# Kernel tuning notes

Measured on AMD Instinct MI355X. Metric: run time of the kernel, lower is better.

## Reference

```python
import jax, jax.numpy as jnp
import numpy as np

N_NODES = 100000
N_EDGES = 6400000


def setup_inputs() -> dict:
    key = jax.random.key(0)
    k1, k2, k3, k4, k5, k6 = jax.random.split(key, 6)
    x = jax.random.normal(k1, (N_NODES, 20), dtype=jnp.float32)
    edge_index = jax.random.randint(k2, (2, N_EDGES), 0, N_NODES, dtype=jnp.int64)
    # Glorot-style init for GCNConv weights, zero bias (PyG default)
    W1 = jax.random.normal(k3, (20, 16), dtype=jnp.float32) * (1.0 / np.sqrt(20))
    b1 = jnp.zeros((16,), dtype=jnp.float32)
    W2 = jax.random.normal(k4, (16, 2), dtype=jnp.float32) * (1.0 / np.sqrt(16))
    b2 = jnp.zeros((2,), dtype=jnp.float32)
    return {"x": x, "edge_index": edge_index, "W1": W1, "b1": b1, "W2": W2, "b2": b2}


def gcn_conv(x, row, col, W, b, num_nodes):
    # x' = D^{-1/2} (A + I) D^{-1/2} X W + b  (PyG GCNConv with self-loops)
    xw = x @ W  # [N, out]
    ones = jnp.ones_like(row, dtype=xw.dtype)
    deg = jax.ops.segment_sum(ones, row, num_segments=num_nodes)  # [N]
    dinv = jnp.where(deg > 0, jax.lax.rsqrt(deg), 0.0)
    norm = dinv[row] * dinv[col]  # [E+N]
    msg = xw[col] * norm[:, None]  # gather + scale
    out = jax.ops.segment_sum(msg, row, num_segments=num_nodes)  # scatter-add
    return out + b


def reference(x, edge_index, W1, b1, W2, b2):
    num_nodes = x.shape[0]
    self_loops = jnp.arange(num_nodes, dtype=edge_index.dtype)
    row = jnp.concatenate([edge_index[0], self_loops])  # target nodes
    col = jnp.concatenate([edge_index[1], self_loops])  # source nodes
    h = gcn_conv(x, row, col, W1, b1, num_nodes)
    h = jax.nn.relu(h)
    # F.dropout(x, training=self.training): identity in eval mode
    h = gcn_conv(h, row, col, W2, b2, num_nodes)
    return jax.nn.log_softmax(h, axis=1)
```

## Files before the change

### kernel.cpp

```cpp
#include <hip/hip_runtime.h>
#include <math.h>


#define XF 20
#define F1 16
#define F2 2
#define RPB 128
#define KMAX 800
#define KP   784
#define TILE 8192
#define EPT 16
#define NJMAX 800
#define CAP 9216
#define BPAD 16

__device__ __forceinline__ unsigned bf16rne(float f) {
    unsigned u = __float_as_uint(f);
    return (u + 0x7FFFu + ((u >> 16) & 1u)) >> 16;
}
__device__ __forceinline__ float bflo(unsigned w) { return __uint_as_float(w << 16); }
__device__ __forceinline__ float bfhi(unsigned w) { return __uint_as_float(w & 0xFFFF0000u); }

__global__ __launch_bounds__(512) void passA_kernel(const int* __restrict__ rows,
                                                    const int* __restrict__ cols,
                                                    int* __restrict__ bhist,
                                                    int* __restrict__ lbt,
                                                    unsigned int* __restrict__ csrtmp,
                                                    int E, int K) {
    __shared__ unsigned int stage[TILE];
    __shared__ int hist[KMAX];
    __shared__ int tsum[512];
    int t = threadIdx.x;
    int bj = blockIdx.x;
    for (int k = t; k < K; k += 512) hist[k] = 0;
    __syncthreads();
    int e0 = bj * TILE;
    int e1 = min(e0 + TILE, E);
    int n = e1 - e0;
    int rloc[EPT];
    #pragma unroll
    for (int it = 0; it < EPT; it++) {
        int e = e0 + it * 512 + t;
        if (e < e1) {
            int r = rows[e];
            rloc[it] = r;
            atomicAdd(&hist[r >> 7], 1);
        }
    }
    __syncthreads();
    int k0 = 2 * t, k1 = 2 * t + 1;
    int v0 = (k0 < K) ? hist[k0] : 0;
    int v1 = (k1 < K) ? hist[k1] : 0;
    int s = v0 + v1;
    tsum[t] = s;
    __syncthreads();
    for (int d = 1; d < 512; d <<= 1) {
        int u = (t >= d) ? tsum[t - d] : 0;
        __syncthreads();
        tsum[t] += u;
        __syncthreads();
    }
    int run = tsum[t] - s;
    long long lrow = (long long)bj * KP;
    if (k0 < K) {
        hist[k0] = run;  lbt[lrow + k0] = run;
        if (v0) atomicAdd(&bhist[k0 * BPAD], v0);
    }
    if (k1 < K) {
        hist[k1] = run + v0;  lbt[lrow + k1] = run + v0;
        if (v1) atomicAdd(&bhist[k1 * BPAD], v1);
    }
    if (t == 0) lbt[lrow + K] = n;
    __syncthreads();
    #pragma unroll
    for (int it = 0; it < EPT; it++) {
        int e = e0 + it * 512 + t;
        if (e < e1) {
            int r = rloc[it];
            int c = cols[e];
            int pos = atomicAdd(&hist[r >> 7], 1);
            stage[pos] = ((unsigned int)c << 7) | (unsigned int)(r & 127);
        }
    }
    __syncthreads();
    for (int ss = t; ss < n; ss += 512)
        csrtmp[(size_t)e0 + ss] = stage[ss];
}

__global__ void bscan_kernel(const int* __restrict__ bhist, int K, int E,
                             int* __restrict__ bbase) {
    __shared__ int tsum[256];
    int t = threadIdx.x;
    int vals[4];
    int s = 0;
    #pragma unroll
    for (int j = 0; j < 4; j++) {
        int idx = t * 4 + j;
        vals[j] = (idx < K) ? bhist[idx * BPAD] : 0;
        s += vals[j];
    }
    tsum[t] = s;
    __syncthreads();
    for (int d = 1; d < 256; d <<= 1) {
        int u = (t >= d) ? tsum[t - d] : 0;
        __syncthreads();
        tsum[t] += u;
        __syncthreads();
    }
    int run = tsum[t] - s;
    #pragma unroll
    for (int j = 0; j < 4; j++) {
        int idx = t * 4 + j;
        if (idx < K) bbase[idx] = run;
        run += vals[j];
    }
    if (t == 0) bbase[K] = E;
}

__global__ __launch_bounds__(512) void passB_kernel(const int* __restrict__ lbt,
                                                    const unsigned int* __restrict__ csrtmp,
                                                    const int* __restrict__ bbase,
                                                    unsigned int* __restrict__ csr,
                                                    int* __restrict__ rowptr,
                                                    float* __restrict__ dinv,
                                                    int N, int K, int E, int nj) {
    __shared__ unsigned int stage[CAP];
    __shared__ int segoff[NJMAX];
    __shared__ int stagepos[NJMAX + 1];
    __shared__ int dcnt[RPB];
    __shared__ int rp[RPB];
    __shared__ int cur[RPB];
    __shared__ int tsum[512];
    int b = blockIdx.x, t = threadIdx.x;
    int lo = b << 7;
    if (t < RPB) { dcnt[t] = 0; cur[t] = 0; }
    int a0 = 2 * t, a1 = 2 * t + 1;
    int la = 0, lb2 = 0;
    if (a0 < nj) {
        const int* lp = lbt + (long long)a0 * KP + b;
        int o0 = lp[0], o1 = lp[1];
        segoff[a0] = o0; la = o1 - o0;
    }
    if (a1 < nj) {
        const int* lp = lbt + (long long)a1 * KP + b;
        int o0 = lp[0], o1 = lp[1];
        segoff[a1] = o0; lb2 = o1 - o0;
    }
    int s = la + lb2;
    tsum[t] = s;
    __syncthreads();
    for (int d = 1; d < 512; d <<= 1) {
        int u = (t >= d) ? tsum[t - d] : 0;
        __syncthreads();
        tsum[t] += u;
        __syncthreads();
    }
    int run = tsum[t] - s;
    if (a0 < nj) stagepos[a0] = run;
    if (a1 < nj) stagepos[a1] = run + la;
    if (t == 511) stagepos[nj] = tsum[511];
    __syncthreads();
    int cnt = min(stagepos[nj], CAP);
    int sw = t >> 3, ln = t & 7;
    for (int seg = sw; seg < nj; seg += 64) {
        int sp = stagepos[seg];
        int len = stagepos[seg + 1] - sp;
        if (sp + len > CAP) len = max(0, CAP - sp);
        size_t src = (size_t)seg * TILE + segoff[seg];
        for (int e2 = ln; e2 < len; e2 += 8) {
            unsigned int p = csrtmp[src + e2];
            stage[sp + e2] = p;
            atomicAdd(&dcnt[p & 127u], 1);
        }
    }
    __syncthreads();
    int gb = bbase[b];
    if (t < 64) {
        int v0 = dcnt[2 * t], v1 = dcnt[2 * t + 1];
        int ss = v0 + v1;
        int sc = ss;
        #pragma unroll
        for (int d = 1; d < 64; d <<= 1) {
            int u = __shfl_up(sc, d);
            if (t >= d) sc += u;
        }
        int excl = gb + sc - ss;
        rp[2 * t] = excl;
        rp[2 * t + 1] = excl + v0;
        int i0 = lo + 2 * t, i1 = i0 + 1;
        if (i0 < N) { rowptr[i0] = excl;      dinv[i0] = rsqrtf((float)v0 + 1.0f); }
        if (i1 < N) { rowptr[i1] = excl + v0; dinv[i1] = rsqrtf((float)v1 + 1.0f); }
        if (t == 0 && b == K - 1) rowptr[N] = E;
    }
    __syncthreads();
    for (int ss = t; ss < cnt; ss += 512) {
        unsigned int p = stage[ss];
        int rr = (int)(p & 127u);
        int dst = rp[rr] + atomicAdd(&cur[rr], 1);
        csr[dst] = p >> 7;
    }
}

__global__ void xw1_kernel(const float* __restrict__ x, const float* __restrict__ W1,
                           const float* __restrict__ dinv, unsigned int* __restrict__ y1h,
                           int N) {
    __shared__ float Ws[XF * F1];
    for (int k = threadIdx.x; k < XF * F1; k += blockDim.x) Ws[k] = W1[k];
    __syncthreads();
    int i = blockIdx.x * blockDim.x + threadIdx.x;
    if (i >= N) return;
    const float4* xv = (const float4*)(x + (size_t)i * XF);
    float xr[XF];
    #pragma unroll
    for (int q = 0; q < 5; q++) {
        float4 v = xv[q];
        xr[q*4+0] = v.x; xr[q*4+1] = v.y; xr[q*4+2] = v.z; xr[q*4+3] = v.w;
    }
    float d = dinv[i];
    float out[F1];
    #pragma unroll
    for (int j = 0; j < F1; j++) {
        float a = 0.f;
        #pragma unroll
        for (int k = 0; k < XF; k++) a += xr[k] * Ws[k * F1 + j];
        out[j] = a * d;
    }
    unsigned int w[8];
    #pragma unroll
    for (int q = 0; q < 8; q++)
        w[q] = bf16rne(out[2*q]) | (bf16rne(out[2*q+1]) << 16);
    uint4* o = (uint4*)(y1h + (size_t)i * 8);
    o[0] = make_uint4(w[0], w[1], w[2], w[3]);
    o[1] = make_uint4(w[4], w[5], w[6], w[7]);
}

__global__ __launch_bounds__(256) void gather16_kernel(const int* __restrict__ rowptr,
                                                       const unsigned int* __restrict__ csr,
                                                       const unsigned int* __restrict__ y1h,
                                                       const float* __restrict__ dinv,
                                                       const float* __restrict__ b1,
                                                       const float* __restrict__ W2,
                                                       float* __restrict__ y2, int N) {
    __shared__ float W2s[F1 * F2];
    if (threadIdx.x < F1 * F2) W2s[threadIdx.x] = W2[threadIdx.x];
    __syncthreads();
    int sub = threadIdx.x >> 5;
    int l = threadIdx.x & 31;
    int i = blockIdx.x * 8 + sub;
    if (i >= N) return;
    int half = l & 1, es = l >> 1;
    int start = rowptr[i], end = rowptr[i + 1];
    const uint4* Y = (const uint4*)y1h;
    float acc[8] = {0.f, 0.f, 0.f, 0.f, 0.f, 0.f, 0.f, 0.f};
    for (int slot = start + es; slot < end; slot += 16) {
        int c = (int)csr[slot];
        uint4 w = Y[(size_t)c * 2 + half];
        acc[0] += bflo(w.x); acc[1] += bfhi(w.x);
        acc[2] += bflo(w.y); acc[3] += bfhi(w.y);
        acc[4] += bflo(w.z); acc[5] += bfhi(w.z);
        acc[6] += bflo(w.w); acc[7] += bfhi(w.w);
    }
    #pragma unroll
    for (int m = 2; m <= 16; m <<= 1) {
        #pragma unroll
        for (int k = 0; k < 8; k++) acc[k] += __shfl_xor(acc[k], m);
    }
    if (l < 2) {
        float d = dinv[i];
        uint4 w = Y[(size_t)i * 2 + l];
        float self[8] = { bflo(w.x), bfhi(w.x), bflo(w.y), bfhi(w.y),
                          bflo(w.z), bfhi(w.z), bflo(w.w), bfhi(w.w) };
        float4 bl = ((const float4*)b1)[l * 2];
        float4 bh = ((const float4*)b1)[l * 2 + 1];
        float bb[8] = { bl.x, bl.y, bl.z, bl.w, bh.x, bh.y, bh.z, bh.w };
        float p0 = 0.f, p1 = 0.f;
        #pragma unroll
        for (int k = 0; k < 8; k++) {
            float hv = fmaxf(d * (acc[k] + self[k]) + bb[k], 0.f);
            p0 += hv * W2s[(l * 8 + k) * 2];
            p1 += hv * W2s[(l * 8 + k) * 2 + 1];
        }
        float q0 = __shfl_xor(p0, 1);
        float q1 = __shfl_xor(p1, 1);
        if (l == 0)
            ((float2*)y2)[i] = make_float2((p0 + q0) * d, (p1 + q1) * d);
    }
}

__global__ __launch_bounds__(256) void gather2_kernel(const int* __restrict__ rowptr,
                                                      const unsigned int* __restrict__ csr,
                                                      const float* __restrict__ y2,
                                                      const float* __restrict__ dinv,
                                                      const float* __restrict__ b2,
                                                      float* __restrict__ out, int N) {
    int sub = threadIdx.x >> 5;
    int l = threadIdx.x & 31;
    int i = blockIdx.x * 8 + sub;
    if (i >= N) return;
    int start = rowptr[i], end = rowptr[i + 1];
    float a0 = 0.f, a1 = 0.f;
    for (int slot = start + l; slot < end; slot += 32) {
        int c = (int)csr[slot];
        float2 v = ((const float2*)y2)[c];
        a0 += v.x;
        a1 += v.y;
    }
    #pragma unroll
    for (int m = 16; m > 0; m >>= 1) {
        a0 += __shfl_xor(a0, m);
        a1 += __shfl_xor(a1, m);
    }
    if (l == 0) {
        float d = dinv[i];
        float2 yi = ((const float2*)y2)[i];
        float v0 = d * (a0 + yi.x) + b2[0];
        float v1 = d * (a1 + yi.y) + b2[1];
        float mm = fmaxf(v0, v1);
        float lse = mm + logf(expf(v0 - mm) + expf(v1 - mm));
        ((float2*)out)[i] = make_float2(v0 - lse, v1 - lse);
    }
}

static inline size_t align256(size_t x) { return (x + 255) & ~(size_t)255; }

extern "C" void kernel_launch(void* const* d_in, const int* in_sizes, int n_in,
                              void* d_out, int out_size, void* d_ws, size_t ws_size,
                              hipStream_t stream) {
    const float* x  = (const float*)d_in[0];
    const int*   ei = (const int*)d_in[1];
    const float* W1 = (const float*)d_in[2];
    const float* b1 = (const float*)d_in[3];
    const float* W2 = (const float*)d_in[4];
    const float* b2 = (const float*)d_in[5];
    float* out = (float*)d_out;

    const int N = in_sizes[0] / XF;
    const int E = in_sizes[1] / 2;
    const int* rows = ei;
    const int* cols = ei + E;
    const int K = (N + RPB - 1) >> 7;
    const int nj = (E + TILE - 1) / TILE;

    char* ws = (char*)d_ws;
    size_t off = 0;
    int*   bhist   = (int*)(ws + off);   off = align256(off + (size_t)KMAX * BPAD * 4);
    size_t zero_bytes = off;
    int*   bbase   = (int*)(ws + off);   off = align256(off + (size_t)(KMAX + 1) * 4);
    int*   rowptr  = (int*)(ws + off);   off = align256(off + (size_t)(N + 1) * 4);
    float* dinv    = (float*)(ws + off); off = align256(off + (size_t)N * 4);
    int*   lbt     = (int*)(ws + off);   off = align256(off + (size_t)nj * KP * 4);
    unsigned int* csr = (unsigned int*)(ws + off); off = align256(off + (size_t)E * 4);
    size_t tmp0 = off;
    unsigned int* csrtmp = (unsigned int*)(ws + tmp0);
    unsigned int* y1h = (unsigned int*)(ws + tmp0);
    float* y2 = (float*)(ws + align256(tmp0 + (size_t)N * 8 * 4));

    hipMemsetAsync(d_ws, 0, zero_bytes, stream);

    const int B = 256;
    const int nbN = (N + B - 1) / B;
    const int nbW = (N + 7) / 8;

    passA_kernel<<<nj, 512, 0, stream>>>(rows, cols, bhist, lbt, csrtmp, E, K);
    bscan_kernel<<<1, B, 0, stream>>>(bhist, K, E, bbase);
    passB_kernel<<<K, 512, 0, stream>>>(lbt, csrtmp, bbase, csr, rowptr, dinv, N, K, E, nj);
    xw1_kernel<<<nbN, B, 0, stream>>>(x, W1, dinv, y1h, N);
    gather16_kernel<<<nbW, B, 0, stream>>>(rowptr, csr, y1h, dinv, b1, W2, y2, N);
    gather2_kernel<<<nbW, B, 0, stream>>>(rowptr, csr, y2, dinv, b2, out, N);
}
```

Baseline: 278.7 us.

## Drop global bucket scan by using fixed per-bucket CSR slots and start/end row pairs

Removes the bucket histogram atomics, the single-block bscan kernel and the memset by giving every 128-row bucket a fixed CAP-sized slot in the CSR array, with rows addressed through (start,end) int2 pairs. passA now uses 1024-thread blocks over 16384-edge tiles, which halves the number of tiles that passB has to merge. Both gather kernels prefetch the next column index one iteration ahead. The cost is a padded CSR buffer, and it depends on no bucket ever holding more than CAP edges, which the random test inputs satisfy.

```diff
diff --git a/kernel.cpp b/kernel.cpp
--- a/kernel.cpp
+++ b/kernel.cpp
@@ -8,11 +8,10 @@
 #define RPB 128
 #define KMAX 800
 #define KP   784
-#define TILE 8192
+#define TILE 16384
 #define EPT 16
-#define NJMAX 800
+#define NJMAX 400
 #define CAP 9216
-#define BPAD 16
 
 __device__ __forceinline__ unsigned bf16rne(float f) {
     unsigned u = __float_as_uint(f);
@@ -21,18 +20,17 @@
 __device__ __forceinline__ float bflo(unsigned w) { return __uint_as_float(w << 16); }
 __device__ __forceinline__ float bfhi(unsigned w) { return __uint_as_float(w & 0xFFFF0000u); }
 
-__global__ __launch_bounds__(512) void passA_kernel(const int* __restrict__ rows,
-                                                    const int* __restrict__ cols,
-                                                    int* __restrict__ bhist,
-                                                    int* __restrict__ lbt,
-                                                    unsigned int* __restrict__ csrtmp,
-                                                    int E, int K) {
+__global__ __launch_bounds__(1024, 8) void passA_kernel(const int* __restrict__ rows,
+                                                        const int* __restrict__ cols,
+                                                        int* __restrict__ lbt,
+                                                        unsigned int* __restrict__ csrtmp,
+                                                        int E, int K) {
     __shared__ unsigned int stage[TILE];
     __shared__ int hist[KMAX];
-    __shared__ int tsum[512];
+    __shared__ int tsum[1024];
     int t = threadIdx.x;
     int bj = blockIdx.x;
-    for (int k = t; k < K; k += 512) hist[k] = 0;
+    for (int k = t; k < K; k += 1024) hist[k] = 0;
     __syncthreads();
     int e0 = bj * TILE;
     int e1 = min(e0 + TILE, E);
@@ -40,7 +38,7 @@
     int rloc[EPT];
     #pragma unroll
     for (int it = 0; it < EPT; it++) {
-        int e = e0 + it * 512 + t;
+        int e = e0 + it * 1024 + t;
         if (e < e1) {
             int r = rows[e];
             rloc[it] = r;
@@ -48,33 +46,23 @@
         }
     }
     __syncthreads();
-    int k0 = 2 * t, k1 = 2 * t + 1;
-    int v0 = (k0 < K) ? hist[k0] : 0;
-    int v1 = (k1 < K) ? hist[k1] : 0;
-    int s = v0 + v1;
-    tsum[t] = s;
-    __syncthreads();
-    for (int d = 1; d < 512; d <<= 1) {
+    int v = (t < K) ? hist[t] : 0;
+    tsum[t] = v;
+    __syncthreads();
+    for (int d = 1; d < 1024; d <<= 1) {
         int u = (t >= d) ? tsum[t - d] : 0;
         __syncthreads();
         tsum[t] += u;
         __syncthreads();
     }
-    int run = tsum[t] - s;
+    int run = tsum[t] - v;
     long long lrow = (long long)bj * KP;
-    if (k0 < K) {
-        hist[k0] = run;  lbt[lrow + k0] = run;
-        if (v0) atomicAdd(&bhist[k0 * BPAD], v0);
-    }
-    if (k1 < K) {
-        hist[k1] = run + v0;  lbt[lrow + k1] = run + v0;
-        if (v1) atomicAdd(&bhist[k1 * BPAD], v1);
-    }
+    if (t < K) { hist[t] = run; lbt[lrow + t] = run; }
     if (t == 0) lbt[lrow + K] = n;
     __syncthreads();
     #pragma unroll
     for (int it = 0; it < EPT; it++) {
-        int e = e0 + it * 512 + t;
+        int e = e0 + it * 1024 + t;
         if (e < e1) {
             int r = rloc[it];
             int c = cols[e];
@@ -83,47 +71,16 @@
         }
     }
     __syncthreads();
-    for (int ss = t; ss < n; ss += 512)
+    for (int ss = t; ss < n; ss += 1024)
         csrtmp[(size_t)e0 + ss] = stage[ss];
-}
-
-__global__ void bscan_kernel(const int* __restrict__ bhist, int K, int E,
-                             int* __restrict__ bbase) {
-    __shared__ int tsum[256];
-    int t = threadIdx.x;
-    int vals[4];
-    int s = 0;
-    #pragma unroll
-    for (int j = 0; j < 4; j++) {
-        int idx = t * 4 + j;
-        vals[j] = (idx < K) ? bhist[idx * BPAD] : 0;
-        s += vals[j];
-    }
-    tsum[t] = s;
-    __syncthreads();
-    for (int d = 1; d < 256; d <<= 1) {
-        int u = (t >= d) ? tsum[t - d] : 0;
-        __syncthreads();
-        tsum[t] += u;
-        __syncthreads();
-    }
-    int run = tsum[t] - s;
-    #pragma unroll
-    for (int j = 0; j < 4; j++) {
-        int idx = t * 4 + j;
-        if (idx < K) bbase[idx] = run;
-        run += vals[j];
-    }
-    if (t == 0) bbase[K] = E;
 }
 
 __global__ __launch_bounds__(512) void passB_kernel(const int* __restrict__ lbt,
                                                     const unsigned int* __restrict__ csrtmp,
-                                                    const int* __restrict__ bbase,
                                                     unsigned int* __restrict__ csr,
-                                                    int* __restrict__ rowptr,
+                                                    int2* __restrict__ rp2,
                                                     float* __restrict__ dinv,
-                                                    int N, int K, int E, int nj) {
+                                                    int N, int K, int nj) {
     __shared__ unsigned int stage[CAP];
     __shared__ int segoff[NJMAX];
     __shared__ int stagepos[NJMAX + 1];
@@ -134,20 +91,13 @@
     int b = blockIdx.x, t = threadIdx.x;
     int lo = b << 7;
     if (t < RPB) { dcnt[t] = 0; cur[t] = 0; }
-    int a0 = 2 * t, a1 = 2 * t + 1;
-    int la = 0, lb2 = 0;
-    if (a0 < nj) {
-        const int* lp = lbt + (long long)a0 * KP + b;
+    int la = 0;
+    if (t < nj) {
+        const int* lp = lbt + (long long)t * KP + b;
         int o0 = lp[0], o1 = lp[1];
-        segoff[a0] = o0; la = o1 - o0;
-    }
-    if (a1 < nj) {
-        const int* lp = lbt + (long long)a1 * KP + b;
-        int o0 = lp[0], o1 = lp[1];
-        segoff[a1] = o0; lb2 = o1 - o0;
-    }
-    int s = la + lb2;
-    tsum[t] = s;
+        segoff[t] = o0; la = o1 - o0;
+    }
+    tsum[t] = la;
     __syncthreads();
     for (int d = 1; d < 512; d <<= 1) {
         int u = (t >= d) ? tsum[t - d] : 0;
@@ -155,9 +105,8 @@
         tsum[t] += u;
         __syncthreads();
     }
-    int run = tsum[t] - s;
-    if (a0 < nj) stagepos[a0] = run;
-    if (a1 < nj) stagepos[a1] = run + la;
+    int run = tsum[t] - la;
+    if (t < nj) stagepos[t] = run;
     if (t == 511) stagepos[nj] = tsum[511];
     __syncthreads();
     int cnt = min(stagepos[nj], CAP);
@@ -174,7 +123,7 @@
         }
     }
     __syncthreads();
-    int gb = bbase[b];
+    int gb = b * CAP;
     if (t < 64) {
         int v0 = dcnt[2 * t], v1 = dcnt[2 * t + 1];
         int ss = v0 + v1;
@@ -188,9 +137,15 @@
         rp[2 * t] = excl;
         rp[2 * t + 1] = excl + v0;
         int i0 = lo + 2 * t, i1 = i0 + 1;
-        if (i0 < N) { rowptr[i0] = excl;      dinv[i0] = rsqrtf((float)v0 + 1.0f); }
-        if (i1 < N) { rowptr[i1] = excl + v0; dinv[i1] = rsqrtf((float)v1 + 1.0f); }
-        if (t == 0 && b == K - 1) rowptr[N] = E;
+        if (i1 < N) {
+            ((int4*)rp2)[(lo >> 1) + t] =
+                make_int4(excl, excl + v0, excl + v0, excl + v0 + v1);
+            dinv[i0] = rsqrtf((float)v0 + 1.0f);
+            dinv[i1] = rsqrtf((float)v1 + 1.0f);
+        } else if (i0 < N) {
+            rp2[i0] = make_int2(excl, excl + v0);
+            dinv[i0] = rsqrtf((float)v0 + 1.0f);
+        }
     }
     __syncthreads();
     for (int ss = t; ss < cnt; ss += 512) {
@@ -234,7 +189,7 @@
     o[1] = make_uint4(w[4], w[5], w[6], w[7]);
 }
 
-__global__ __launch_bounds__(256) void gather16_kernel(const int* __restrict__ rowptr,
+__global__ __launch_bounds__(256) void gather16_kernel(const int2* __restrict__ rp2,
                                                        const unsigned int* __restrict__ csr,
                                                        const unsigned int* __restrict__ y1h,
                                                        const float* __restrict__ dinv,
@@ -249,16 +204,21 @@
     int i = blockIdx.x * 8 + sub;
     if (i >= N) return;
     int half = l & 1, es = l >> 1;
-    int start = rowptr[i], end = rowptr[i + 1];
+    int2 se = rp2[i];
+    int start = se.x, end = se.y;
     const uint4* Y = (const uint4*)y1h;
     float acc[8] = {0.f, 0.f, 0.f, 0.f, 0.f, 0.f, 0.f, 0.f};
-    for (int slot = start + es; slot < end; slot += 16) {
-        int c = (int)csr[slot];
+    int slot = start + es;
+    int c = (slot < end) ? (int)csr[slot] : 0;
+    while (slot < end) {
+        int ns = slot + 16;
+        int cn = (ns < end) ? (int)csr[ns] : 0;
         uint4 w = Y[(size_t)c * 2 + half];
         acc[0] += bflo(w.x); acc[1] += bfhi(w.x);
         acc[2] += bflo(w.y); acc[3] += bfhi(w.y);
         acc[4] += bflo(w.z); acc[5] += bfhi(w.z);
         acc[6] += bflo(w.w); acc[7] += bfhi(w.w);
+        c = cn; slot = ns;
     }
     #pragma unroll
     for (int m = 2; m <= 16; m <<= 1) {
@@ -287,7 +247,7 @@
     }
 }
 
-__global__ __launch_bounds__(256) void gather2_kernel(const int* __restrict__ rowptr,
+__global__ __launch_bounds__(256) void gather2_kernel(const int2* __restrict__ rp2,
                                                       const unsigned int* __restrict__ csr,
                                                       const float* __restrict__ y2,
                                                       const float* __restrict__ dinv,
@@ -297,13 +257,18 @@
     int l = threadIdx.x & 31;
     int i = blockIdx.x * 8 + sub;
     if (i >= N) return;
-    int start = rowptr[i], end = rowptr[i + 1];
+    int2 se = rp2[i];
+    int start = se.x, end = se.y;
     float a0 = 0.f, a1 = 0.f;
-    for (int slot = start + l; slot < end; slot += 32) {
-        int c = (int)csr[slot];
+    int slot = start + l;
+    int c = (slot < end) ? (int)csr[slot] : 0;
+    while (slot < end) {
+        int ns = slot + 32;
+        int cn = (ns < end) ? (int)csr[ns] : 0;
         float2 v = ((const float2*)y2)[c];
         a0 += v.x;
         a1 += v.y;
+        c = cn; slot = ns;
     }
     #pragma unroll
     for (int m = 16; m > 0; m >>= 1) {
@@ -343,28 +308,23 @@
 
     char* ws = (char*)d_ws;
     size_t off = 0;
-    int*   bhist   = (int*)(ws + off);   off = align256(off + (size_t)KMAX * BPAD * 4);
-    size_t zero_bytes = off;
-    int*   bbase   = (int*)(ws + off);   off = align256(off + (size_t)(KMAX + 1) * 4);
-    int*   rowptr  = (int*)(ws + off);   off = align256(off + (size_t)(N + 1) * 4);
+    int2*  rp2     = (int2*)(ws + off);  off = align256(off + (size_t)N * 8);
     float* dinv    = (float*)(ws + off); off = align256(off + (size_t)N * 4);
     int*   lbt     = (int*)(ws + off);   off = align256(off + (size_t)nj * KP * 4);
-    unsigned int* csr = (unsigned int*)(ws + off); off = align256(off + (size_t)E * 4);
+    unsigned int* csr = (unsigned int*)(ws + off);
+    off = align256(off + (size_t)K * CAP * 4);
     size_t tmp0 = off;
     unsigned int* csrtmp = (unsigned int*)(ws + tmp0);
     unsigned int* y1h = (unsigned int*)(ws + tmp0);
     float* y2 = (float*)(ws + align256(tmp0 + (size_t)N * 8 * 4));
 
-    hipMemsetAsync(d_ws, 0, zero_bytes, stream);
-
     const int B = 256;
     const int nbN = (N + B - 1) / B;
     const int nbW = (N + 7) / 8;
 
-    passA_kernel<<<nj, 512, 0, stream>>>(rows, cols, bhist, lbt, csrtmp, E, K);
-    bscan_kernel<<<1, B, 0, stream>>>(bhist, K, E, bbase);
-    passB_kernel<<<K, 512, 0, stream>>>(lbt, csrtmp, bbase, csr, rowptr, dinv, N, K, E, nj);
+    passA_kernel<<<nj, 1024, 0, stream>>>(rows, cols, lbt, csrtmp, E, K);
+    passB_kernel<<<K, 512, 0, stream>>>(lbt, csrtmp, csr, rp2, dinv, N, K, nj);
     xw1_kernel<<<nbN, B, 0, stream>>>(x, W1, dinv, y1h, N);
-    gather16_kernel<<<nbW, B, 0, stream>>>(rowptr, csr, y1h, dinv, b1, W2, y2, N);
-    gather2_kernel<<<nbW, B, 0, stream>>>(rowptr, csr, y2, dinv, b2, out, N);
-}
+    gather16_kernel<<<nbW, B, 0, stream>>>(rp2, csr, y1h, dinv, b1, W2, y2, N);
+    gather2_kernel<<<nbW, B, 0, stream>>>(rp2, csr, y2, dinv, b2, out, N);
+}
```

Result: faster. 240.4 us (-13.7%).
